# Optimization experiments

Hardware: AMD Instinct MI355X
Metric: run time of the kernel (lower is better)

Reference implementation:

```python
import jax, jax.numpy as jnp
import numpy as np

B, N, D, H = 8, 2048, 512, 8  # batch, seq (incl. CLS), emb_dim, heads


def setup_inputs() -> dict:
    key = jax.random.key(0)
    kx, km, k1, k2, k3, k4 = jax.random.split(key, 6)
    x = jax.random.normal(kx, (B, N, D), dtype=jnp.float32)
    # mask covers the N-1 non-CLS tokens; forward pads a leading True for CLS
    mask = jax.random.bernoulli(km, p=0.9, shape=(B, N - 1))
    s = 0.02
    Wqkv = jax.random.normal(k1, (D, 3 * D), dtype=jnp.float32) * s
    bqkv = jax.random.normal(k2, (3 * D,), dtype=jnp.float32) * s
    Wout = jax.random.normal(k3, (D, D), dtype=jnp.float32) * s
    bout = jax.random.normal(k4, (D,), dtype=jnp.float32) * s
    return {"x": x, "mask": mask, "Wqkv": Wqkv, "bqkv": bqkv,
            "Wout": Wout, "bout": bout, "num_heads": H}


def reference(x, mask, Wqkv, bqkv, Wout, bout, num_heads):
    b, n, d = x.shape
    h = num_heads
    dh = d // h
    scale = d ** (-0.5)  # NOTE: module scales by emb_dim^-0.5, not head_dim^-0.5

    qkv = x @ Wqkv + bqkv                      # [b, n, 3d]
    q, k, v = jnp.split(qkv, 3, axis=-1)
    def to_heads(t):
        return t.reshape(b, n, h, dh).transpose(0, 2, 1, 3)  # [b, h, n, dh]
    q, k, v = map(to_heads, (q, k, v))

    scores = jnp.einsum('bhqd,bhkd->bhqk', q, k) * scale     # [b, h, n, n]

    # pad leading True for CLS token, then outer-product pair mask
    m = jnp.pad(mask, ((0, 0), (1, 0)), constant_values=True)  # [b, n]
    pair = m[:, None, :, None] & m[:, None, None, :]           # [b, 1, n, n]
    neg = jnp.asarray(-1e9, dtype=scores.dtype)  # finite stand-in for -inf (avoids NaN rows)
    scores = jnp.where(pair, scores, neg)

    attn = jax.nn.softmax(scores, axis=-1)
    out = jnp.einsum('bhqk,bhkd->bhqd', attn, v)               # [b, h, n, dh]
    out = out.transpose(0, 2, 1, 3).reshape(b, n, d)
    return out @ Wout + bout
```

## Files before the change

### kernel.cpp

```cpp
#include <hip/hip_runtime.h>
#include <math.h>

#define BB  8
#define SEQ 2048
#define EMB 512
#define NH  8
#define DH  64
#define NBH (BB * NH)
#define MROWS (BB * SEQ)
#define QKV_ELEMS ((size_t)NBH * SEQ * DH)
#define MASK_ELEMS (BB * (SEQ - 1))
#define QSCALE 0.06375871307545f

typedef __attribute__((ext_vector_type(8)))  short short8;
typedef __attribute__((ext_vector_type(4)))  float float4e;
typedef __attribute__((ext_vector_type(16))) float float16e;
typedef __attribute__((ext_vector_type(4)))  unsigned int uint4e;
typedef __attribute__((ext_vector_type(2)))  unsigned int uint2e;
typedef unsigned short ushort_t;

static __device__ inline unsigned short f2bf(float f) {
    unsigned int u = __float_as_uint(f);
    unsigned int r = (u + 0x7fffu + ((u >> 16) & 1u)) >> 16;
    return (unsigned short)r;
}

static __device__ inline void gl_lds16(const unsigned short* g, unsigned short* l) {
    __builtin_amdgcn_global_load_lds(
        (const __attribute__((address_space(1))) void*)g,
        (__attribute__((address_space(3))) void*)l, 16, 0, 0);
}

#define PREP_CONV   8192
#define PREP_MASK   (PREP_CONV + 64)
#define PREP_WQ     (PREP_MASK + (1536 / 32) * (EMB / 32))
#define PREP_TOTAL  (PREP_WQ + (EMB / 32) * (EMB / 32))

__global__ __launch_bounds__(256) void prep(const float* __restrict__ x,
                                            const void* __restrict__ mraw,
                                            const float* __restrict__ Wqkv,
                                            const float* __restrict__ Wout,
                                            ushort_t* __restrict__ xb,
                                            float* __restrict__ pmf,
                                            float* __restrict__ mkl,
                                            float* __restrict__ zrow,
                                            ushort_t* __restrict__ wqt,
                                            ushort_t* __restrict__ wot) {
    __shared__ float T[32][33];
    __shared__ int flag;
    const int bid = blockIdx.x;
    const int tid = threadIdx.x;

    if (bid < PREP_CONV) {
        const size_t i = ((size_t)bid * 256 + tid) * 4;
        float4 v = *(const float4*)&x[i];
        ushort4 o;
        o.x = f2bf(v.x); o.y = f2bf(v.y); o.z = f2bf(v.z); o.w = f2bf(v.w);
        *(ushort4*)&xb[i] = o;
    } else if (bid < PREP_MASK) {
        if (tid == 0) flag = 0;
        __syncthreads();
        const unsigned int* mi = (const unsigned int*)mraw;
        int local = 0;
        for (int i = tid; i < MASK_ELEMS / 4; i += 256) {
            if (mi[i] > 1u) local = 1;
        }
        if (local) flag = 1;
        __syncthreads();
        const int isbyte = flag;
        const unsigned char* mb = (const unsigned char*)mraw;
        const int* m32 = (const int*)mraw;
        const int i = (bid - PREP_CONV) * 256 + tid;
        const int b = i >> 11, n = i & (SEQ - 1);
        int v;
        if (n == 0) v = 1;
        else {
            const int src = b * (SEQ - 1) + n - 1;
            v = isbyte ? (int)mb[src] : (m32[src] != 0 ? 1 : 0);
        }
        pmf[i] = v ? 1.0f : 0.0f;
        mkl[i] = v ? 0.0f : -1e9f;
        if (i < SEQ) zrow[i] = 0.0f;
    } else {
        const float* src;
        ushort_t* dst;
        int N, idx;
        if (bid < PREP_WQ) {
            src = Wqkv; dst = wqt; N = 1536; idx = bid - PREP_MASK;
        } else {
            src = Wout; dst = wot; N = EMB; idx = bid - PREP_WQ;
        }
        const int nb = N / 32;
        const int n0 = (idx % nb) * 32;
        const int k0 = (idx / nb) * 32;
        {
            const int r = tid >> 3, c4 = (tid & 7) * 4;
            *(float4*)&T[r][c4] = *(const float4*)&src[(size_t)(k0 + r) * N + n0 + c4];
        }
        __syncthreads();
        const int n = tid >> 3, k4 = (tid & 7) * 4;
        ushort4 hv;
        hv.x = f2bf(T[k4 + 0][n]);
        hv.y = f2bf(T[k4 + 1][n]);
        hv.z = f2bf(T[k4 + 2][n]);
        hv.w = f2bf(T[k4 + 3][n]);
        *(ushort4*)&dst[(size_t)(n0 + n) * EMB + k0 + k4] = hv;
    }
}

__global__ __launch_bounds__(256) void qkv_mfma(const ushort_t* __restrict__ xb,
                                                const ushort_t* __restrict__ wt,
                                                const float* __restrict__ bias,
                                                ushort_t* __restrict__ qb,
                                                ushort_t* __restrict__ kb,
                                                ushort_t* __restrict__ vt) {
    __shared__ __align__(16) ushort_t As[128 * 64];
    __shared__ __align__(16) ushort_t Bs[128 * 64];
    const int tid  = threadIdx.x;
    const int w    = tid >> 6;
    const int lane = tid & 63;
    const int l16  = lane & 15;
    const int quad = lane >> 4;
    const int wq   = w >> 1;
    const int wn   = w & 1;
    const int bid  = blockIdx.x;
    const int c    = bid & 7;
    const int r    = bid >> 3;
    const int mloc = r / 12;
    const int nblk = r - mloc * 12;
    const int row0 = (c * 16 + mloc) * 128;
    const int col0 = nblk * 128;

    float4e acc[4][4];
    #pragma unroll
    for (int i = 0; i < 4; ++i)
        #pragma unroll
        for (int j = 0; j < 4; ++j) acc[i][j] = (float4e){0.f, 0.f, 0.f, 0.f};

    const int srow = tid >> 3;
    const int csrc = (tid & 7) ^ (srow & 7);

    for (int k0 = 0; k0 < EMB; k0 += 64) {
        #pragma unroll
        for (int s = 0; s < 4; ++s) {
            const int row = s * 32 + srow;
            gl_lds16(xb + (size_t)(row0 + row) * EMB + k0 + csrc * 8,
                     As + s * 2048 + w * 512);
            gl_lds16(wt + (size_t)(col0 + row) * EMB + k0 + csrc * 8,
                     Bs + s * 2048 + w * 512);
        }
        __syncthreads();
        #pragma unroll
        for (int kk = 0; kk < 2; ++kk) {
            short8 af[4], bf[4];
            #pragma unroll
            for (int mt = 0; mt < 4; ++mt) {
                const int rm = wq * 64 + mt * 16 + l16;
                af[mt] = *(const short8*)(As + rm * 64 + (((kk * 4 + quad) ^ (rm & 7)) * 8));
            }
            #pragma unroll
            for (int nt = 0; nt < 4; ++nt) {
                const int rn = wn * 64 + nt * 16 + l16;
                bf[nt] = *(const short8*)(Bs + rn * 64 + (((kk * 4 + quad) ^ (rn & 7)) * 8));
            }
            #pragma unroll
            for (int mt = 0; mt < 4; ++mt)
                #pragma unroll
                for (int nt = 0; nt < 4; ++nt)
                    acc[mt][nt] = __builtin_amdgcn_mfma_f32_16x16x32_bf16(af[mt], bf[nt], acc[mt][nt], 0, 0, 0);
        }
        __syncthreads();
    }

    #pragma unroll
    for (int nt = 0; nt < 4; ++nt) {
        const int cb    = col0 + wn * 64 + nt * 16;
        const int which = cb >> 9;
        const int h     = (cb >> 6) & 7;
        const int dcol  = (cb & 63) + l16;
        const float bz  = bias[cb + l16];
        if (which == 2) {
            #pragma unroll
            for (int mt = 0; mt < 4; ++mt) {
                const int rg = row0 + wq * 64 + mt * 16 + quad * 4;
                const int b = rg >> 11, n = rg & (SEQ - 1);
                ushort4 ov;
                ov.x = f2bf(acc[mt][nt][0] + bz);
                ov.y = f2bf(acc[mt][nt][1] + bz);
                ov.z = f2bf(acc[mt][nt][2] + bz);
                ov.w = f2bf(acc[mt][nt][3] + bz);
                *(ushort4*)&vt[((size_t)(b * NH + h) * DH + dcol) * SEQ + n] = ov;
            }
        } else {
            ushort_t* base = (which == 0) ? qb : kb;
            const float sc = (which == 0) ? QSCALE : 1.0f;
            #pragma unroll
            for (int mt = 0; mt < 4; ++mt) {
                #pragma unroll
                for (int i = 0; i < 4; ++i) {
                    const int rg = row0 + wq * 64 + mt * 16 + quad * 4 + i;
                    const int b = rg >> 11;
                    const int n = rg & (SEQ - 1);
                    base[((size_t)(b * NH + h) * SEQ + n) * DH + dcol] =
                        f2bf((acc[mt][nt][i] + bz) * sc);
                }
            }
        }
    }
}

__device__ inline void stage_tile(const ushort_t* kbh, const ushort_t* vbh, int kt,
                                  ushort_t* Kd, ushort_t* Vd,
                                  const int* crow, const int* csoff, int wbase) {
    #pragma unroll
    for (int j = 0; j < 4; ++j) {
        gl_lds16(kbh + (size_t)(kt * 64 + crow[j]) * DH + csoff[j],
                 Kd + (j * 128 + wbase) * 8);
        gl_lds16(vbh + (size_t)crow[j] * SEQ + kt * 64 + csoff[j],
                 Vd + (j * 128 + wbase) * 8);
    }
}

__global__ __launch_bounds__(128, 2) void attn_mfma(const ushort_t* __restrict__ qb,
                                                    const ushort_t* __restrict__ kb,
                                                    const ushort_t* __restrict__ vt,
                                                    const float* __restrict__ pmf,
                                                    const float* __restrict__ mkl,
                                                    const float* __restrict__ zrow,
                                                    ushort_t* __restrict__ ab) {
    __shared__ __align__(16) ushort_t Ks[2][64 * 64];
    __shared__ __align__(16) ushort_t Vts[2][64 * 64];
    __shared__ float lw[2][64];

    const int tid = threadIdx.x;
    const int w   = tid >> 6;
    const int lane = tid & 63;
    const int l5  = lane & 31;
    const int h   = lane >> 5;
    const int bid = blockIdx.x;
    const int ord = bid >> 3;
    const int bh  = (bid & 7) * 8 + (ord >> 4);
    const int qt  = ord & 15;
    const int b   = bh >> 3;
    const int hh  = bh & 7;
    const int q0  = qt * 128 + w * 64;

    const ushort_t* qbh = qb + (size_t)bh * SEQ * DH;
    short8 qf[2][4];
    #pragma unroll
    for (int t = 0; t < 2; ++t)
        #pragma unroll
        for (int kc = 0; kc < 4; ++kc)
            qf[t][kc] = *(const short8*)(qbh + (size_t)(q0 + t * 32 + l5) * DH + kc * 16 + h * 8);

    const float* crb[2];
    #pragma unroll
    for (int t = 0; t < 2; ++t) {
        const float mq = pmf[b * SEQ + q0 + t * 32 + l5];
        if (mq == 0.0f) {
            const short8 z8 = {0, 0, 0, 0, 0, 0, 0, 0};
            #pragma unroll
            for (int kc = 0; kc < 4; ++kc) qf[t][kc] = z8;
        }
        crb[t] = (mq != 0.0f) ? (mkl + b * SEQ) : zrow;
    }

    int crow[4], csoff[4];
    #pragma unroll
    for (int j = 0; j < 4; ++j) {
        const int c = j * 128 + tid;
        crow[j]  = c >> 3;
        csoff[j] = ((c & 7) ^ (crow[j] & 7)) * 8;
    }
    const int wbase = w * 64;
    const ushort_t* kbh = kb + (size_t)bh * SEQ * DH;
    const ushort_t* vbh = vt + (size_t)bh * DH * SEQ;

    float16e o[2][2];
    #pragma unroll
    for (int t = 0; t < 2; ++t)
        #pragma unroll
        for (int d = 0; d < 2; ++d) o[t][d] = (float16e)0.0f;
    float l_i[2] = {0.f, 0.f};

    stage_tile(kbh, vbh, 0, Ks[0], Vts[0], crow, csoff, wbase);

    for (int kt = 0; kt < 32; ++kt) {
        __syncthreads();
        const int cur = kt & 1;
        if (kt < 31)
            stage_tile(kbh, vbh, kt + 1, Ks[cur ^ 1], Vts[cur ^ 1], crow, csoff, wbase);

        #pragma unroll
        for (int s = 0; s < 2; ++s) {
            float16e st[2];
            #pragma unroll
            for (int t = 0; t < 2; ++t) {
                #pragma unroll
                for (int g2 = 0; g2 < 4; ++g2) {
                    const float4e c4 = *(const float4e*)(crb[t] + kt * 64 + s * 32 + g2 * 8 + h * 4);
                    #pragma unroll
                    for (int j = 0; j < 4; ++j)
                        st[t][g2 * 4 + j] = c4[j];
                }
            }

            const int krow = s * 32 + l5;
            short8 kf[4];
            #pragma unroll
            for (int kc = 0; kc < 4; ++kc)
                kf[kc] = *(const short8*)(Ks[cur] + krow * 64 + (((kc * 2 + h) ^ (krow & 7)) * 8));
            __builtin_amdgcn_s_setprio(1);
            #pragma unroll
            for (int kc = 0; kc < 4; ++kc) {
                st[0] = __builtin_amdgcn_mfma_f32_32x32x16_bf16(kf[kc], qf[0][kc], st[0], 0, 0, 0);
                st[1] = __builtin_amdgcn_mfma_f32_32x32x16_bf16(kf[kc], qf[1][kc], st[1], 0, 0, 0);
            }
            __builtin_amdgcn_s_setprio(0);

            short8 af[2][2];
            #pragma unroll
            for (int t = 0; t < 2; ++t) {
                unsigned int a[8];
                float lacc = 0.f;
                #pragma unroll
                for (int j = 0; j < 8; ++j) {
                    const float p0 = __builtin_amdgcn_exp2f(st[t][2 * j]);
                    const float p1 = __builtin_amdgcn_exp2f(st[t][2 * j + 1]);
                    lacc += p0 + p1;
                    a[j] = (__float_as_uint(p0) >> 16) | (__float_as_uint(p1) & 0xffff0000u);
                }
                l_i[t] += lacc;
                #pragma unroll
                for (int c = 0; c < 2; ++c) {
                    const uint2e r02 = __builtin_amdgcn_permlane32_swap(a[4 * c],     a[4 * c + 2], false, false);
                    const uint2e r13 = __builtin_amdgcn_permlane32_swap(a[4 * c + 1], a[4 * c + 3], false, false);
                    uint4e fv;
                    fv.x = r02[0];
                    fv.y = r13[0];
                    fv.z = r02[1];
                    fv.w = r13[1];
                    af[t][c] = __builtin_bit_cast(short8, fv);
                }
            }

            __builtin_amdgcn_s_setprio(1);
            #pragma unroll
            for (int c = 0; c < 2; ++c) {
                #pragma unroll
                for (int d = 0; d < 2; ++d) {
                    const int vrow = d * 32 + l5;
                    const short8 vf = *(const short8*)(Vts[cur] + vrow * 64 +
                                       (((s * 4 + c * 2 + h) ^ (vrow & 7)) * 8));
                    o[0][d] = __builtin_amdgcn_mfma_f32_32x32x16_bf16(af[0][c], vf, o[0][d], 0, 0, 0);
                    o[1][d] = __builtin_amdgcn_mfma_f32_32x32x16_bf16(af[1][c], vf, o[1][d], 0, 0, 0);
                }
            }
            __builtin_amdgcn_s_setprio(0);
        }
    }

    #pragma unroll
    for (int t = 0; t < 2; ++t) {
        const float l = l_i[t] + __shfl_xor(l_i[t], 32);
        lw[w][t * 32 + l5] = l;
    }

    ushort_t* ob = ab + ((size_t)b * SEQ + q0) * EMB + hh * DH;
    #pragma unroll
    for (int t = 0; t < 2; ++t) {
        #pragma unroll
        for (int r = 0; r < 16; ++r) {
            const int ql = (r & 3) + 8 * (r >> 2) + 4 * h;
            const float inv = 1.0f / lw[w][t * 32 + ql];
            #pragma unroll
            for (int d = 0; d < 2; ++d)
                ob[(size_t)(t * 32 + ql) * EMB + d * 32 + l5] = f2bf(o[t][d][r] * inv);
        }
    }
}

__global__ __launch_bounds__(256) void out_mfma(const ushort_t* __restrict__ ab,
                                                const ushort_t* __restrict__ wot,
                                                const float* __restrict__ bias,
                                                float* __restrict__ out) {
    __shared__ __align__(16) ushort_t As[128 * 64];
    __shared__ __align__(16) ushort_t Bs[128 * 64];
    const int tid  = threadIdx.x;
    const int w    = tid >> 6;
    const int lane = tid & 63;
    const int l16  = lane & 15;
    const int quad = lane >> 4;
    const int wq   = w >> 1;
    const int wn   = w & 1;
    const int bid  = blockIdx.x;
    const int c    = bid & 7;
    const int r    = bid >> 3;
    const int mloc = r >> 2;
    const int nblk = r & 3;
    const int row0 = (c * 16 + mloc) * 128;
    const int col0 = nblk * 128;

    float4e acc[4][4];
    #pragma unroll
    for (int i = 0; i < 4; ++i)
        #pragma unroll
        for (int j = 0; j < 4; ++j) acc[i][j] = (float4e){0.f, 0.f, 0.f, 0.f};

    const int srow = tid >> 3;
    const int csrc = (tid & 7) ^ (srow & 7);

    for (int k0 = 0; k0 < EMB; k0 += 64) {
        #pragma unroll
        for (int s = 0; s < 4; ++s) {
            const int row = s * 32 + srow;
            gl_lds16(ab + (size_t)(row0 + row) * EMB + k0 + csrc * 8,
                     As + s * 2048 + w * 512);
            gl_lds16(wot + (size_t)(col0 + row) * EMB + k0 + csrc * 8,
                     Bs + s * 2048 + w * 512);
        }
        __syncthreads();
        #pragma unroll
        for (int kk = 0; kk < 2; ++kk) {
            short8 af[4], bf[4];
            #pragma unroll
            for (int mt = 0; mt < 4; ++mt) {
                const int rm = wq * 64 + mt * 16 + l16;
                af[mt] = *(const short8*)(As + rm * 64 + (((kk * 4 + quad) ^ (rm & 7)) * 8));
            }
            #pragma unroll
            for (int nt = 0; nt < 4; ++nt) {
                const int rn = wn * 64 + nt * 16 + l16;
                bf[nt] = *(const short8*)(Bs + rn * 64 + (((kk * 4 + quad) ^ (rn & 7)) * 8));
            }
            #pragma unroll
            for (int mt = 0; mt < 4; ++mt)
                #pragma unroll
                for (int nt = 0; nt < 4; ++nt)
                    acc[mt][nt] = __builtin_amdgcn_mfma_f32_16x16x32_bf16(af[mt], bf[nt], acc[mt][nt], 0, 0, 0);
        }
        __syncthreads();
    }

    #pragma unroll
    for (int nt = 0; nt < 4; ++nt) {
        const int col_g = col0 + wn * 64 + nt * 16 + l16;
        const float bz = bias[col_g];
        #pragma unroll
        for (int mt = 0; mt < 4; ++mt) {
            #pragma unroll
            for (int i = 0; i < 4; ++i) {
                const int row_g = row0 + wq * 64 + mt * 16 + quad * 4 + i;
                out[(size_t)row_g * EMB + col_g] = acc[mt][nt][i] + bz;
            }
        }
    }
}

extern "C" void kernel_launch(void* const* d_in, const int* in_sizes, int n_in,
                              void* d_out, int out_size, void* d_ws, size_t ws_size,
                              hipStream_t stream) {
    const float* x    = (const float*)d_in[0];
    const void*  mask = d_in[1];
    const float* Wqkv = (const float*)d_in[2];
    const float* bqkv = (const float*)d_in[3];
    const float* Wout = (const float*)d_in[4];
    const float* bout = (const float*)d_in[5];
    float* out = (float*)d_out;

    ushort_t* xb  = (ushort_t*)d_ws;
    ushort_t* wqt = xb + (size_t)MROWS * EMB;
    ushort_t* wot = wqt + (size_t)1536 * EMB;
    ushort_t* qb  = wot + (size_t)EMB * EMB;
    ushort_t* kb  = qb + QKV_ELEMS;
    ushort_t* vt  = kb + QKV_ELEMS;
    ushort_t* ab  = vt + QKV_ELEMS;
    float*    pmf = (float*)(ab + (size_t)MROWS * EMB);
    float*    mkl = pmf + (size_t)BB * SEQ;
    float*    zrw = mkl + (size_t)BB * SEQ;

    prep<<<dim3(PREP_TOTAL), 256, 0, stream>>>(x, mask, Wqkv, Wout, xb, pmf, mkl, zrw, wqt, wot);
    qkv_mfma<<<dim3(1536), 256, 0, stream>>>(xb, wqt, bqkv, qb, kb, vt);
    attn_mfma<<<dim3(NBH * (SEQ / 128)), 128, 0, stream>>>(qb, kb, vt, pmf, mkl, zrw, ab);
    out_mfma<<<dim3(512), 256, 0, stream>>>(ab, wot, bout, out);
}
```

Measured before the change: 248.9 us.

## Use single-wave attention blocks with bitmask key masking and barrier-free staging

```diff
diff --git a/kernel.cpp b/kernel.cpp
--- a/kernel.cpp
+++ b/kernel.cpp
@@ -42,8 +42,7 @@
                                             const float* __restrict__ Wout,
                                             ushort_t* __restrict__ xb,
                                             float* __restrict__ pmf,
-                                            float* __restrict__ mkl,
-                                            float* __restrict__ zrow,
+                                            unsigned* __restrict__ pmb,
                                             ushort_t* __restrict__ wqt,
                                             ushort_t* __restrict__ wot) {
     __shared__ float T[32][33];
@@ -79,8 +78,8 @@
             v = isbyte ? (int)mb[src] : (m32[src] != 0 ? 1 : 0);
         }
         pmf[i] = v ? 1.0f : 0.0f;
-        mkl[i] = v ? 0.0f : -1e9f;
-        if (i < SEQ) zrow[i] = 0.0f;
+        const unsigned long long bl = __ballot(v);
+        if ((tid & 31) == 0) pmb[i >> 5] = (unsigned)(bl >> (tid & 32));
     } else {
         const float* src;
         ushort_t* dst;
@@ -209,41 +208,28 @@
     }
 }
 
-__device__ inline void stage_tile(const ushort_t* kbh, const ushort_t* vbh, int kt,
-                                  ushort_t* Kd, ushort_t* Vd,
-                                  const int* crow, const int* csoff, int wbase) {
-    #pragma unroll
-    for (int j = 0; j < 4; ++j) {
-        gl_lds16(kbh + (size_t)(kt * 64 + crow[j]) * DH + csoff[j],
-                 Kd + (j * 128 + wbase) * 8);
-        gl_lds16(vbh + (size_t)crow[j] * SEQ + kt * 64 + csoff[j],
-                 Vd + (j * 128 + wbase) * 8);
-    }
-}
-
-__global__ __launch_bounds__(128, 2) void attn_mfma(const ushort_t* __restrict__ qb,
-                                                    const ushort_t* __restrict__ kb,
-                                                    const ushort_t* __restrict__ vt,
-                                                    const float* __restrict__ pmf,
-                                                    const float* __restrict__ mkl,
-                                                    const float* __restrict__ zrow,
-                                                    ushort_t* __restrict__ ab) {
-    __shared__ __align__(16) ushort_t Ks[2][64 * 64];
-    __shared__ __align__(16) ushort_t Vts[2][64 * 64];
-    __shared__ float lw[2][64];
-
-    const int tid = threadIdx.x;
-    const int w   = tid >> 6;
-    const int lane = tid & 63;
-    const int l5  = lane & 31;
-    const int h   = lane >> 5;
+__global__ __launch_bounds__(64, 2) void attn_mfma(const ushort_t* __restrict__ qb,
+                                                   const ushort_t* __restrict__ kb,
+                                                   const ushort_t* __restrict__ vt,
+                                                   const float* __restrict__ pmf,
+                                                   const unsigned* __restrict__ pmb,
+                                                   ushort_t* __restrict__ ab) {
+    __shared__ __align__(16) ushort_t Ks0[32 * 64];
+    __shared__ __align__(16) ushort_t Vs0[64 * 32];
+    __shared__ __align__(16) ushort_t Ks1[32 * 64];
+    __shared__ __align__(16) ushort_t Vs1[64 * 32];
+    __shared__ float lw[64];
+
+    const int lane = threadIdx.x;
+    const int l5   = lane & 31;
+    const int h    = lane >> 5;
     const int bid = blockIdx.x;
     const int ord = bid >> 3;
-    const int bh  = (bid & 7) * 8 + (ord >> 4);
-    const int qt  = ord & 15;
+    const int bh  = (bid & 7) * 8 + (ord >> 5);
+    const int qt  = ord & 31;
     const int b   = bh >> 3;
     const int hh  = bh & 7;
-    const int q0  = qt * 128 + w * 64;
+    const int q0  = qt * 64;
 
     const ushort_t* qbh = qb + (size_t)bh * SEQ * DH;
     short8 qf[2][4];
@@ -253,29 +239,28 @@
         for (int kc = 0; kc < 4; ++kc)
             qf[t][kc] = *(const short8*)(qbh + (size_t)(q0 + t * 32 + l5) * DH + kc * 16 + h * 8);
 
-    const float* crb[2];
+    bool qv[2];
     #pragma unroll
     for (int t = 0; t < 2; ++t) {
         const float mq = pmf[b * SEQ + q0 + t * 32 + l5];
-        if (mq == 0.0f) {
+        qv[t] = (mq != 0.0f);
+        if (!qv[t]) {
             const short8 z8 = {0, 0, 0, 0, 0, 0, 0, 0};
             #pragma unroll
             for (int kc = 0; kc < 4; ++kc) qf[t][kc] = z8;
         }
-        crb[t] = (mq != 0.0f) ? (mkl + b * SEQ) : zrow;
-    }
-
-    int crow[4], csoff[4];
-    #pragma unroll
-    for (int j = 0; j < 4; ++j) {
-        const int c = j * 128 + tid;
-        crow[j]  = c >> 3;
-        csoff[j] = ((c & 7) ^ (crow[j] & 7)) * 8;
-    }
-    const int wbase = w * 64;
+    }
+
+    const unsigned wm = pmb[b * 64 + lane];
+
     const ushort_t* kbh = kb + (size_t)bh * SEQ * DH;
     const ushort_t* vbh = vt + (size_t)bh * DH * SEQ;
 
+    const int l3  = lane >> 3;
+    const int c8  = (lane & 7) ^ (l3 & 7);
+    const int l2  = lane >> 2;
+    const int c4v = (lane & 3) ^ (l2 & 3);
+
     float16e o[2][2];
     #pragma unroll
     for (int t = 0; t < 2; ++t)
@@ -283,87 +268,94 @@
         for (int d = 0; d < 2; ++d) o[t][d] = (float16e)0.0f;
     float l_i[2] = {0.f, 0.f};
 
-    stage_tile(kbh, vbh, 0, Ks[0], Vts[0], crow, csoff, wbase);
-
-    for (int kt = 0; kt < 32; ++kt) {
-        __syncthreads();
-        const int cur = kt & 1;
-        if (kt < 31)
-            stage_tile(kbh, vbh, kt + 1, Ks[cur ^ 1], Vts[cur ^ 1], crow, csoff, wbase);
-
-        #pragma unroll
-        for (int s = 0; s < 2; ++s) {
-            float16e st[2];
-            #pragma unroll
-            for (int t = 0; t < 2; ++t) {
-                #pragma unroll
-                for (int g2 = 0; g2 < 4; ++g2) {
-                    const float4e c4 = *(const float4e*)(crb[t] + kt * 64 + s * 32 + g2 * 8 + h * 4);
-                    #pragma unroll
-                    for (int j = 0; j < 4; ++j)
-                        st[t][g2 * 4 + j] = c4[j];
-                }
-            }
-
-            const int krow = s * 32 + l5;
-            short8 kf[4];
-            #pragma unroll
-            for (int kc = 0; kc < 4; ++kc)
-                kf[kc] = *(const short8*)(Ks[cur] + krow * 64 + (((kc * 2 + h) ^ (krow & 7)) * 8));
-            __builtin_amdgcn_s_setprio(1);
-            #pragma unroll
-            for (int kc = 0; kc < 4; ++kc) {
-                st[0] = __builtin_amdgcn_mfma_f32_32x32x16_bf16(kf[kc], qf[0][kc], st[0], 0, 0, 0);
-                st[1] = __builtin_amdgcn_mfma_f32_32x32x16_bf16(kf[kc], qf[1][kc], st[1], 0, 0, 0);
-            }
-            __builtin_amdgcn_s_setprio(0);
-
-            short8 af[2][2];
-            #pragma unroll
-            for (int t = 0; t < 2; ++t) {
-                unsigned int a[8];
-                float lacc = 0.f;
-                #pragma unroll
-                for (int j = 0; j < 8; ++j) {
-                    const float p0 = __builtin_amdgcn_exp2f(st[t][2 * j]);
-                    const float p1 = __builtin_amdgcn_exp2f(st[t][2 * j + 1]);
-                    lacc += p0 + p1;
-                    a[j] = (__float_as_uint(p0) >> 16) | (__float_as_uint(p1) & 0xffff0000u);
-                }
-                l_i[t] += lacc;
-                #pragma unroll
-                for (int c = 0; c < 2; ++c) {
-                    const uint2e r02 = __builtin_amdgcn_permlane32_swap(a[4 * c],     a[4 * c + 2], false, false);
-                    const uint2e r13 = __builtin_amdgcn_permlane32_swap(a[4 * c + 1], a[4 * c + 3], false, false);
-                    uint4e fv;
-                    fv.x = r02[0];
-                    fv.y = r13[0];
-                    fv.z = r02[1];
-                    fv.w = r13[1];
-                    af[t][c] = __builtin_bit_cast(short8, fv);
-                }
-            }
-
-            __builtin_amdgcn_s_setprio(1);
+    auto stage = [&](int kt, ushort_t* Kd, ushort_t* Vd) {
+        #pragma unroll
+        for (int j = 0; j < 4; ++j) {
+            gl_lds16(kbh + (size_t)(kt * 32 + j * 8 + l3) * DH + c8 * 8, Kd + j * 512);
+            gl_lds16(vbh + (size_t)(j * 16 + l2) * SEQ + kt * 32 + c4v * 8, Vd + j * 512);
+        }
+    };
+
+    auto body = [&](int kt, const ushort_t* Kr, const ushort_t* Vr,
+                    ushort_t* Kw, ushort_t* Vw) {
+        stage(kt + 1, Kw, Vw);
+        asm volatile("s_waitcnt vmcnt(8)" ::: "memory");
+        __builtin_amdgcn_sched_barrier(0);
+
+        const unsigned mwf = (unsigned)__builtin_amdgcn_readlane((int)wm, kt);
+        const unsigned mh  = h ? (mwf >> 4) : mwf;
+        float16e st0, st1;
+        #pragma unroll
+        for (int j = 0; j < 16; ++j) {
+            const float bv = (mh & (1u << ((j & 3) + 8 * (j >> 2)))) ? 0.0f : -1e9f;
+            st0[j] = qv[0] ? bv : 0.0f;
+            st1[j] = qv[1] ? bv : 0.0f;
+        }
+
+        short8 kf[4];
+        #pragma unroll
+        for (int kc = 0; kc < 4; ++kc)
+            kf[kc] = *(const short8*)(Kr + l5 * 64 + (((kc * 2 + h) ^ (l5 & 7)) * 8));
+        __builtin_amdgcn_s_setprio(1);
+        #pragma unroll
+        for (int kc = 0; kc < 4; ++kc) {
+            st0 = __builtin_amdgcn_mfma_f32_32x32x16_bf16(kf[kc], qf[0][kc], st0, 0, 0, 0);
+            st1 = __builtin_amdgcn_mfma_f32_32x32x16_bf16(kf[kc], qf[1][kc], st1, 0, 0, 0);
+        }
+        __builtin_amdgcn_s_setprio(0);
+
+        short8 af[2][2];
+        #pragma unroll
+        for (int t = 0; t < 2; ++t) {
+            const float16e& st = t ? st1 : st0;
+            unsigned int a[8];
+            float lacc = 0.f;
+            #pragma unroll
+            for (int j = 0; j < 8; ++j) {
+                const float p0 = __builtin_amdgcn_exp2f(st[2 * j]);
+                const float p1 = __builtin_amdgcn_exp2f(st[2 * j + 1]);
+                lacc += p0 + p1;
+                a[j] = (__float_as_uint(p0) >> 16) | (__float_as_uint(p1) & 0xffff0000u);
+            }
+            l_i[t] += lacc;
             #pragma unroll
             for (int c = 0; c < 2; ++c) {
-                #pragma unroll
-                for (int d = 0; d < 2; ++d) {
-                    const int vrow = d * 32 + l5;
-                    const short8 vf = *(const short8*)(Vts[cur] + vrow * 64 +
-                                       (((s * 4 + c * 2 + h) ^ (vrow & 7)) * 8));
-                    o[0][d] = __builtin_amdgcn_mfma_f32_32x32x16_bf16(af[0][c], vf, o[0][d], 0, 0, 0);
-                    o[1][d] = __builtin_amdgcn_mfma_f32_32x32x16_bf16(af[1][c], vf, o[1][d], 0, 0, 0);
-                }
-            }
-            __builtin_amdgcn_s_setprio(0);
-        }
+                const uint2e r02 = __builtin_amdgcn_permlane32_swap(a[4 * c],     a[4 * c + 2], false, false);
+                const uint2e r13 = __builtin_amdgcn_permlane32_swap(a[4 * c + 1], a[4 * c + 3], false, false);
+                uint4e fv;
+                fv.x = r02[0];
+                fv.y = r13[0];
+                fv.z = r02[1];
+                fv.w = r13[1];
+                af[t][c] = __builtin_bit_cast(short8, fv);
+            }
+        }
+
+        __builtin_amdgcn_s_setprio(1);
+        #pragma unroll
+        for (int c = 0; c < 2; ++c) {
+            #pragma unroll
+            for (int d = 0; d < 2; ++d) {
+                const int vr = d * 32 + l5;
+                const short8 vf = *(const short8*)(Vr + vr * 32 +
+                                   (((c * 2 + h) ^ (vr & 3)) * 8));
+                o[0][d] = __builtin_amdgcn_mfma_f32_32x32x16_bf16(af[0][c], vf, o[0][d], 0, 0, 0);
+                o[1][d] = __builtin_amdgcn_mfma_f32_32x32x16_bf16(af[1][c], vf, o[1][d], 0, 0, 0);
+            }
+        }
+        __builtin_amdgcn_s_setprio(0);
+    };
+
+    stage(0, Ks0, Vs0);
+    for (int kt2 = 0; kt2 < 64; kt2 += 2) {
+        body(kt2,     Ks0, Vs0, Ks1, Vs1);
+        body(kt2 + 1, Ks1, Vs1, Ks0, Vs0);
     }
 
     #pragma unroll
     for (int t = 0; t < 2; ++t) {
         const float l = l_i[t] + __shfl_xor(l_i[t], 32);
-        lw[w][t * 32 + l5] = l;
+        lw[t * 32 + l5] = l;
     }
 
     ushort_t* ob = ab + ((size_t)b * SEQ + q0) * EMB + hh * DH;
@@ -372,7 +364,7 @@
         #pragma unroll
         for (int r = 0; r < 16; ++r) {
             const int ql = (r & 3) + 8 * (r >> 2) + 4 * h;
-            const float inv = 1.0f / lw[w][t * 32 + ql];
+            const float inv = 1.0f / lw[t * 32 + ql];
             #pragma unroll
             for (int d = 0; d < 2; ++d)
                 ob[(size_t)(t * 32 + ql) * EMB + d * 32 + l5] = f2bf(o[t][d][r] * inv);
@@ -476,11 +468,10 @@
     ushort_t* vt  = kb + QKV_ELEMS;
     ushort_t* ab  = vt + QKV_ELEMS;
     float*    pmf = (float*)(ab + (size_t)MROWS * EMB);
-    float*    mkl = pmf + (size_t)BB * SEQ;
-    float*    zrw = mkl + (size_t)BB * SEQ;
-
-    prep<<<dim3(PREP_TOTAL), 256, 0, stream>>>(x, mask, Wqkv, Wout, xb, pmf, mkl, zrw, wqt, wot);
+    unsigned* pmb = (unsigned*)(pmf + (size_t)BB * SEQ);
+
+    prep<<<dim3(PREP_TOTAL), 256, 0, stream>>>(x, mask, Wqkv, Wout, xb, pmf, pmb, wqt, wot);
     qkv_mfma<<<dim3(1536), 256, 0, stream>>>(xb, wqt, bqkv, qb, kb, vt);
-    attn_mfma<<<dim3(NBH * (SEQ / 128)), 128, 0, stream>>>(qb, kb, vt, pmf, mkl, zrw, ab);
+    attn_mfma<<<dim3(NBH * (SEQ / 64)), 64, 0, stream>>>(qb, kb, vt, pmf, pmb, ab);
     out_mfma<<<dim3(512), 256, 0, stream>>>(ab, wot, bout, out);
 }
```

Result: no change. 247.1 us (-0.7%).
